# Kernel optimization log

Hardware: AMD Instinct MI355X
Metric: run time of the kernel (lower is better)

## Reference

```python
import jax, jax.numpy as jnp
import numpy as np
from jax import lax

B, H, W = 128, 128, 128
CHANS = [3, 32, 64, 128]   # convolution_structure
F, FH, FW = 128, 16, 16    # n_features, feature map size after 3 maxpools
P = FH * FW                # flatten_feature_size = 256
E, OUT = 32, 53            # expert_output_len, output_len


def _conv(x, w, b):
    # NCHW conv, 3x3, SAME padding, stride 1
    y = lax.conv_general_dilated(x, w, (1, 1), 'SAME',
                                 dimension_numbers=('NCHW', 'OIHW', 'NCHW'))
    return y + b[None, :, None, None]


def _maxpool2(x):
    return lax.reduce_window(x, -jnp.inf, lax.max,
                             (1, 1, 2, 2), (1, 1, 2, 2), 'VALID')


def setup_inputs() -> dict:
    key = jax.random.key(0)
    ks = jax.random.split(key, 16)

    def n(k, shape, fan_in):
        return jax.random.normal(k, shape, jnp.float32) / np.float32(np.sqrt(fan_in))

    inp = {'x': jax.random.normal(ks[0], (B, CHANS[0], H, W), jnp.float32)}
    for i in range(3):
        cin, cout = CHANS[i], CHANS[i + 1]
        inp[f'cw{i + 1}'] = n(ks[1 + i], (cout, cin, 3, 3), cin * 9)
        inp[f'cb{i + 1}'] = jnp.zeros((cout,), jnp.float32)
    inp['Wa'] = n(ks[4], (F, P), P)
    inp['ba'] = jnp.zeros((F,), jnp.float32)
    # per-expert MLP 256 -> 256 -> 128 -> 32 (128 experts, batched)
    inp['ew1'] = n(ks[5], (F, 256, 256), 256)
    inp['eb1'] = jnp.zeros((F, 256), jnp.float32)
    inp['ew2'] = n(ks[6], (F, 256, 128), 256)
    inp['eb2'] = jnp.zeros((F, 128), jnp.float32)
    inp['ew3'] = n(ks[7], (F, 128, E), 128)
    inp['eb3'] = jnp.zeros((F, E), jnp.float32)
    inp['fw'] = n(ks[8], (F * E, OUT), F * E)
    inp['fb'] = jnp.zeros((OUT,), jnp.float32)
    return inp


def reference(x, cw1, cb1, cw2, cb2, cw3, cb3, Wa, ba,
              ew1, eb1, ew2, eb2, ew3, eb3, fw, fb):
    # CNNBlock: (conv3x3 + ReLU + maxpool2) x 3  -> [B, F, 16, 16]
    h = x
    for w, b in ((cw1, cb1), (cw2, cb2), (cw3, cb3)):
        h = _maxpool2(jax.nn.relu(_conv(h, w, b)))
    feat = h.reshape(h.shape[0], F, P)                        # [B, F, 256]

    # AttentionBlock: per-feature scalar gate (attention_value = 1)
    att = jax.nn.sigmoid(jnp.einsum('bfp,fp->bf', feat, Wa) + ba)[:, :, None]

    # Experts: 128 independent gated MLPs, batched as grouped GEMMs
    z = feat * att                                            # input gating
    z = jax.nn.relu(jnp.einsum('bfp,fpq->bfq', z, ew1) + eb1)
    z = jax.nn.relu(jnp.einsum('bfp,fpq->bfq', z, ew2) + eb2)
    z = jnp.einsum('bfp,fpq->bfq', z, ew3) + eb3              # [B, F, 32]

    # outer ReLU over stacked expert outputs, flatten, final dense (att=1)
    z = jax.nn.relu(z).reshape(z.shape[0], -1)                # [B, 4096]
    return z @ fw + fb                                        # [B, 53]
```

## Files before the change

kernel.cpp:

```cpp
#include <hip/hip_runtime.h>
#include <hip/hip_bf16.h>
#include <math.h>

#define NF 128
#define NP 256

typedef __attribute__((ext_vector_type(8))) short bf16x8;
typedef __attribute__((ext_vector_type(4))) short bf16x4;
typedef __attribute__((ext_vector_type(4))) float f32x4;

#define GLOBAL_AS __attribute__((address_space(1)))
#define LDS_AS __attribute__((address_space(3)))

__global__ void __launch_bounds__(256) wpack_k(const float* __restrict__ w,
                                               __hip_bfloat16* __restrict__ wp,
                                               int COUT, int CIN)
{
    int i = blockIdx.x * 256 + threadIdx.x;
    int total = 9 * COUT * CIN;
    if (i >= total) return;
    int o  = i / (COUT * CIN);
    int r  = i - o * (COUT * CIN);
    int co = r / CIN, ci = r - co * CIN;
    wp[i] = __float2bfloat16(w[(size_t)(co * CIN + ci) * 9 + o]);
}

__global__ void __launch_bounds__(256) wpack1_k(const float* __restrict__ w,
                                                __hip_bfloat16* __restrict__ wp1)
{
    int i = blockIdx.x * 256 + threadIdx.x;
    if (i >= 2048) return;
    int s = i >> 10, co = (i >> 5) & 31, k = i & 31;
    int o = s * 8 + (k >> 2), ch = k & 3;
    float v = 0.f;
    if (o < 9 && ch < 3) v = w[(size_t)(co * 3 + ch) * 9 + o];
    wp1[i] = __float2bfloat16(v);
}

__global__ void __launch_bounds__(256) tpack_k(const float* __restrict__ in,
                                               __hip_bfloat16* __restrict__ out,
                                               int P, int Q, int qtiles)
{
    const int f  = blockIdx.y;
    const int pt = blockIdx.x / qtiles, qt = blockIdx.x - pt * qtiles;
    __shared__ float t[32][33];
    const float* src = in + (size_t)f * P * Q;
    __hip_bfloat16* dst = out + (size_t)f * P * Q;
    const int rr = threadIdx.x >> 5, c = threadIdx.x & 31;
    #pragma unroll
    for (int i = 0; i < 4; ++i)
        t[rr + i * 8][c] = src[(size_t)(pt * 32 + rr + i * 8) * Q + qt * 32 + c];
    __syncthreads();
    #pragma unroll
    for (int i = 0; i < 4; ++i)
        dst[(size_t)(qt * 32 + rr + i * 8) * P + pt * 32 + c] =
            __float2bfloat16(t[c][rr + i * 8]);
}

__global__ void __launch_bounds__(256) fwt_k(const float* __restrict__ fw, float* __restrict__ fwt)
{
    int i = blockIdx.x * 256 + threadIdx.x;
    if (i >= 53 * 4096) return;
    int o = i >> 12, k = i & 4095;
    fwt[i] = fw[(size_t)k * 53 + o];
}

__global__ void __launch_bounds__(256, 2) conv1_mfma(
    const float* __restrict__ x,
    const __hip_bfloat16* __restrict__ wp1,
    const float* __restrict__ bias,
    __hip_bfloat16* __restrict__ out)
{
    __shared__ char lds[14 * 130 * 8];
    const int rb  = blockIdx.x * 8;
    const int b   = blockIdx.z;
    const int tid = threadIdx.x;

    #pragma unroll
    for (int t = 0; t < 8; ++t) {
        int u = tid + t * 256;
        if (u < 14 * 130) {
            int px = u % 130, row = u / 130;
            int gy = rb + row - 1, gx = px - 1;
            unsigned short hv[4] = {0, 0, 0, 0};
            if (gy >= 0 && gy < 128 && gx >= 0 && gx < 128) {
                size_t base = (((size_t)b * 3) * 128 + gy) * 128 + gx;
                __hip_bfloat16 h0 = __float2bfloat16(x[base]);
                __hip_bfloat16 h1 = __float2bfloat16(x[base + 16384]);
                __hip_bfloat16 h2 = __float2bfloat16(x[base + 32768]);
                __builtin_memcpy(&hv[0], &h0, 2);
                __builtin_memcpy(&hv[1], &h1, 2);
                __builtin_memcpy(&hv[2], &h2, 2);
            }
            *(int2*)(lds + u * 8) = *(const int2*)hv;
        }
    }
    __syncthreads();

    const int w = tid >> 6, lane = tid & 63, p = lane & 15, q = lane >> 4;

    f32x4 acc[16][2];
    #pragma unroll
    for (int m = 0; m < 16; ++m)
        #pragma unroll
        for (int n = 0; n < 2; ++n) {
            acc[m][n][0] = 0.f; acc[m][n][1] = 0.f;
            acc[m][n][2] = 0.f; acc[m][n][3] = 0.f;
        }

    #pragma unroll
    for (int s = 0; s < 2; ++s) {
        bf16x8 bfr[2];
        #pragma unroll
        for (int n = 0; n < 2; ++n)
            bfr[n] = *(const bf16x8*)(wp1 + (size_t)(s * 32 + n * 16 + p) * 32 + q * 8);
        const int o0 = s * 8 + q * 2, o1 = o0 + 1;
        const int dy0 = o0 / 3, dx0 = o0 - 3 * dy0;
        const int dy1 = o1 / 3, dx1 = o1 - 3 * dy1;
        #pragma unroll
        for (int m = 0; m < 16; ++m) {
            const int mr = m >> 3, mx = m & 7;
            const int r0 = (2 * w + mr + dy0) * 130 + mx * 16 + p + dx0;
            const int r1 = (2 * w + mr + dy1) * 130 + mx * 16 + p + dx1;
            bf16x4 lo = *(const bf16x4*)(lds + r0 * 8);
            bf16x4 hi = *(const bf16x4*)(lds + r1 * 8);
            bf16x8 afr = __builtin_shufflevector(lo, hi, 0, 1, 2, 3, 4, 5, 6, 7);
            #pragma unroll
            for (int n = 0; n < 2; ++n)
                acc[m][n] = __builtin_amdgcn_mfma_f32_16x16x32_bf16(afr, bfr[n], acc[m][n], 0, 0, 0);
        }
    }

    const int prow = (rb >> 1) + w;
    float bv[2] = { bias[p], bias[16 + p] };
    #pragma unroll
    for (int mx = 0; mx < 8; ++mx)
        #pragma unroll
        for (int n = 0; n < 2; ++n) {
            f32x4 lo = acc[mx][n], hi = acc[8 + mx][n];
            float v0 = fmaxf(fmaxf(fmaxf(lo[0], lo[1]), fmaxf(hi[0], hi[1])) + bv[n], 0.f);
            float v1 = fmaxf(fmaxf(fmaxf(lo[2], lo[3]), fmaxf(hi[2], hi[3])) + bv[n], 0.f);
            int px = mx * 8 + q * 2;
            size_t base = ((size_t)(b * 64 + prow) * 64 + px) * 32 + n * 16 + p;
            out[base]      = __float2bfloat16(v0);
            out[base + 32] = __float2bfloat16(v1);
        }
}

template<int W, int CIN, int COUT, int SWZ, int OUTF>
__global__ void __launch_bounds__(256, 2) conv_mfma(
    const __hip_bfloat16* __restrict__ in,
    const __hip_bfloat16* __restrict__ wp,
    const float* __restrict__ bias,
    __hip_bfloat16* __restrict__ outb,
    float* __restrict__ outf)
{
    constexpr int XW  = W / 16;
    constexpr int AF  = 2 * XW;
    constexpr int BF  = COUT / 16;
    constexpr int CH  = CIN / 8;
    constexpr int KH  = CIN / 32;
    constexpr int NSTEP = 9 * KH;
    constexpr int PXW = W + 2;
    constexpr int UNITS  = 10 * PXW * CH;
    constexpr int NIT    = (UNITS + 255) / 256;
    constexpr int STAGEB = UNITS * 16;
    constexpr int OUTLDS = OUTF ? (COUT * 68 * 4) : 0;
    constexpr int LDSB   = STAGEB > OUTLDS ? STAGEB : OUTLDS;

    __shared__ int4 ldsv[(LDSB + 15) / 16];
    char* ldsc = (char*)ldsv;

    const int rb  = blockIdx.x * 8;
    const int b   = blockIdx.z;
    const int tid = threadIdx.x;
    const int w = tid >> 6, lane = tid & 63, p = lane & 15, q = lane >> 4;

    #pragma unroll
    for (int t = 0; t < NIT; ++t) {
        int u = tid + t * 256;
        if (u < UNITS) {
            int ch = u % CH; int pl = u / CH;
            int xx = pl % PXW; int row = pl / PXW;
            int gy = rb + row - 1, gx = xx - 1;
            if (gy >= 0 && gy < W && gx >= 0 && gx < W) {
                int ch_src = SWZ ? (ch ^ (pl & 7)) : ch;
                const __hip_bfloat16* gp = in + ((size_t)(b * W + gy) * W + gx) * CIN + ch_src * 8;
                char* lb = ldsc + (size_t)(t * 256 + (tid & ~63)) * 16;
                __builtin_amdgcn_global_load_lds(
                    (const GLOBAL_AS void*)gp, (LDS_AS void*)lb, 16, 0, 0);
            } else {
                *(int4*)(ldsc + (size_t)u * 16) = make_int4(0, 0, 0, 0);
            }
        }
    }

    bf16x8 bcur[BF], bnxt[BF];
    #pragma unroll
    for (int n = 0; n < BF; ++n)
        bcur[n] = *(const bf16x8*)(wp + (size_t)(n * 16 + p) * CIN + q * 8);

    __syncthreads();

    f32x4 acc[AF][BF];
    #pragma unroll
    for (int m = 0; m < AF; ++m)
        #pragma unroll
        for (int n = 0; n < BF; ++n) {
            acc[m][n][0] = 0.f; acc[m][n][1] = 0.f;
            acc[m][n][2] = 0.f; acc[m][n][3] = 0.f;
        }

    float bv[BF];
    #pragma unroll
    for (int n = 0; n < BF; ++n) bv[n] = bias[n * 16 + p];

    #pragma unroll 1
    for (int s = 0; s < NSTEP; ++s) {
        const int o  = (KH == 1) ? s : (s >> 1);
        const int h  = (KH == 1) ? 0 : (s & 1);
        const int ky = o / 3, kx = o - 3 * (o / 3);

        if (s + 1 < NSTEP) {
            const int o2 = (KH == 1) ? (s + 1) : ((s + 1) >> 1);
            const int h2 = (KH == 1) ? 0 : ((s + 1) & 1);
            #pragma unroll
            for (int n = 0; n < BF; ++n)
                bnxt[n] = *(const bf16x8*)(wp + (size_t)(o2 * COUT + n * 16 + p) * CIN + h2 * 32 + q * 8);
        }

        bf16x8 afr[AF];
        #pragma unroll
        for (int m = 0; m < AF; ++m) {
            const int mr = m / XW, mx = m % XW;
            const int pix = (2 * w + mr + ky) * PXW + mx * 16 + kx + p;
            const int ch = h * 4 + q;
            const int slot = SWZ ? (pix * CH + (ch ^ (pix & 7))) : (pix * CH + ch);
            afr[m] = *(const bf16x8*)(ldsc + slot * 16);
        }
        #pragma unroll
        for (int m = 0; m < AF; ++m)
            #pragma unroll
            for (int n = 0; n < BF; ++n)
                acc[m][n] = __builtin_amdgcn_mfma_f32_16x16x32_bf16(afr[m], bcur[n], acc[m][n], 0, 0, 0);

        #pragma unroll
        for (int n = 0; n < BF; ++n) bcur[n] = bnxt[n];
    }

    const int prow = (rb >> 1) + w;
    if constexpr (OUTF == 0) {
        #pragma unroll
        for (int mx = 0; mx < XW; ++mx)
            #pragma unroll
            for (int n = 0; n < BF; ++n) {
                f32x4 lo = acc[mx][n], hi = acc[XW + mx][n];
                float v0 = fmaxf(fmaxf(fmaxf(lo[0], lo[1]), fmaxf(hi[0], hi[1])) + bv[n], 0.f);
                float v1 = fmaxf(fmaxf(fmaxf(lo[2], lo[3]), fmaxf(hi[2], hi[3])) + bv[n], 0.f);
                int px = mx * 8 + q * 2;
                size_t base = ((size_t)(b * (W / 2) + prow) * (W / 2) + px) * COUT + n * 16 + p;
                outb[base]        = __float2bfloat16(v0);
                outb[base + COUT] = __float2bfloat16(v1);
            }
    } else {
        __syncthreads();
        float* fl = (float*)ldsc;
        #pragma unroll
        for (int mx = 0; mx < XW; ++mx)
            #pragma unroll
            for (int n = 0; n < BF; ++n) {
                f32x4 lo = acc[mx][n], hi = acc[XW + mx][n];
                float v0 = fmaxf(fmaxf(fmaxf(lo[0], lo[1]), fmaxf(hi[0], hi[1])) + bv[n], 0.f);
                float v1 = fmaxf(fmaxf(fmaxf(lo[2], lo[3]), fmaxf(hi[2], hi[3])) + bv[n], 0.f);
                int px = mx * 8 + q * 2;
                fl[(n * 16 + p) * 68 + w * 16 + px]     = v0;
                fl[(n * 16 + p) * 68 + w * 16 + px + 1] = v1;
            }
        __syncthreads();
        for (int i = tid; i < COUT * 16; i += 256) {
            int c = i >> 4, j4 = i & 15;
            float4 vv = *(const float4*)&fl[c * 68 + j4 * 4];
            *(float4*)(outf + (size_t)(b * COUT + c) * 256 + (rb >> 1) * 16 + j4 * 4) = vv;
        }
    }
}

__global__ void __launch_bounds__(256) attention_k(
    const float* __restrict__ feat, const float* __restrict__ Wa,
    const float* __restrict__ ba, float* __restrict__ att)
{
    const int wid  = blockIdx.x * 4 + (threadIdx.x >> 6);
    const int lane = threadIdx.x & 63;
    const int b = wid >> 7, f = wid & 127;

    const float4 a  = ((const float4*)&feat[((size_t)b * NF + f) * NP])[lane];
    const float4 wv = ((const float4*)&Wa[(size_t)f * NP])[lane];
    float s = a.x * wv.x + a.y * wv.y + a.z * wv.z + a.w * wv.w;
    #pragma unroll
    for (int off = 32; off; off >>= 1) s += __shfl_down(s, off);
    if (lane == 0) att[b * NF + f] = 1.f / (1.f + expf(-(s + ba[f])));
}

__global__ void __launch_bounds__(256, 2) experts_mfma(
    const float* __restrict__ feat, const float* __restrict__ att,
    const __hip_bfloat16* __restrict__ w1, const float* __restrict__ eb1,
    const __hip_bfloat16* __restrict__ w2, const float* __restrict__ eb2,
    const __hip_bfloat16* __restrict__ w3, const float* __restrict__ eb3,
    float* __restrict__ z)
{
    const int f  = blockIdx.x;
    const int r0 = blockIdx.y * 32;
    const int tid = threadIdx.x;

    __shared__ char lds[32768];
    char* Xb  = lds;
    char* H1b = lds + 16384;
    char* H2b = lds;

    for (int u = tid; u < 32 * 32; u += 256) {
        int row = u >> 5, ch = u & 31;
        int b = r0 + row;
        const float* src = feat + ((size_t)b * NF + f) * NP + ch * 8;
        float g = att[b * NF + f];
        float4 v0 = *(const float4*)src;
        float4 v1 = *(const float4*)(src + 4);
        unsigned short hv[8];
        float vv[8] = {v0.x, v0.y, v0.z, v0.w, v1.x, v1.y, v1.z, v1.w};
        #pragma unroll
        for (int j = 0; j < 8; ++j) {
            __hip_bfloat16 hb = __float2bfloat16(vv[j] * g);
            __builtin_memcpy(&hv[j], &hb, 2);
        }
        int slot = row * 32 + (ch ^ (row & 7));
        *(int4*)(Xb + slot * 16) = *(const int4*)hv;
    }
    __syncthreads();

    const int wv = tid >> 6, lane = tid & 63, p = lane & 15, q = lane >> 4;
    const int rh = wv & 1, cf = wv >> 1;
    const int mrow = rh * 16;

    f32x4 acc1[8];
    #pragma unroll
    for (int n = 0; n < 8; ++n) { acc1[n][0]=0.f; acc1[n][1]=0.f; acc1[n][2]=0.f; acc1[n][3]=0.f; }
    #pragma unroll
    for (int k = 0; k < 8; ++k) {
        bf16x8 bfr[8];
        #pragma unroll
        for (int n = 0; n < 8; ++n)
            bfr[n] = *(const bf16x8*)(w1 + ((size_t)f * 256 + cf * 128 + n * 16 + p) * 256 + k * 32 + q * 8);
        int row = mrow + p, ch = k * 4 + q;
        bf16x8 afr = *(const bf16x8*)(Xb + (row * 32 + (ch ^ (row & 7))) * 16);
        #pragma unroll
        for (int n = 0; n < 8; ++n)
            acc1[n] = __builtin_amdgcn_mfma_f32_16x16x32_bf16(afr, bfr[n], acc1[n], 0, 0, 0);
    }
    #pragma unroll
    for (int n = 0; n < 8; ++n) {
        int col = cf * 128 + n * 16 + p;
        float bb = eb1[(size_t)f * 256 + col];
        #pragma unroll
        for (int reg = 0; reg < 4; ++reg) {
            float v = fmaxf(acc1[n][reg] + bb, 0.f);
            int row = mrow + q * 4 + reg;
            int slot = row * 32 + ((col >> 3) ^ (row & 7));
            *(__hip_bfloat16*)(H1b + slot * 16 + (col & 7) * 2) = __float2bfloat16(v);
        }
    }
    __syncthreads();

    f32x4 acc2[4];
    #pragma unroll
    for (int n = 0; n < 4; ++n) { acc2[n][0]=0.f; acc2[n][1]=0.f; acc2[n][2]=0.f; acc2[n][3]=0.f; }
    #pragma unroll
    for (int k = 0; k < 8; ++k) {
        bf16x8 bfr[4];
        #pragma unroll
        for (int n = 0; n < 4; ++n)
            bfr[n] = *(const bf16x8*)(w2 + ((size_t)f * 128 + cf * 64 + n * 16 + p) * 256 + k * 32 + q * 8);
        int row = mrow + p, ch = k * 4 + q;
        bf16x8 afr = *(const bf16x8*)(H1b + (row * 32 + (ch ^ (row & 7))) * 16);
        #pragma unroll
        for (int n = 0; n < 4; ++n)
            acc2[n] = __builtin_amdgcn_mfma_f32_16x16x32_bf16(afr, bfr[n], acc2[n], 0, 0, 0);
    }
    #pragma unroll
    for (int n = 0; n < 4; ++n) {
        int col = cf * 64 + n * 16 + p;
        float bb = eb2[(size_t)f * 128 + col];
        #pragma unroll
        for (int reg = 0; reg < 4; ++reg) {
            float v = fmaxf(acc2[n][reg] + bb, 0.f);
            int row = mrow + q * 4 + reg;
            int slot = row * 16 + ((col >> 3) ^ (row & 7));
            *(__hip_bfloat16*)(H2b + slot * 16 + (col & 7) * 2) = __float2bfloat16(v);
        }
    }
    __syncthreads();

    f32x4 acc3;
    acc3[0]=0.f; acc3[1]=0.f; acc3[2]=0.f; acc3[3]=0.f;
    #pragma unroll
    for (int k = 0; k < 4; ++k) {
        bf16x8 bfr = *(const bf16x8*)(w3 + ((size_t)f * 32 + cf * 16 + p) * 128 + k * 32 + q * 8);
        int row = mrow + p, ch = k * 4 + q;
        bf16x8 afr = *(const bf16x8*)(H2b + (row * 16 + (ch ^ (row & 7))) * 16);
        acc3 = __builtin_amdgcn_mfma_f32_16x16x32_bf16(afr, bfr, acc3, 0, 0, 0);
    }
    {
        float bb = eb3[(size_t)f * 32 + cf * 16 + p];
        #pragma unroll
        for (int reg = 0; reg < 4; ++reg) {
            float v = fmaxf(acc3[reg] + bb, 0.f);
            int row = r0 + mrow + q * 4 + reg;
            z[(size_t)row * 4096 + f * 32 + cf * 16 + p] = v;
        }
    }
}

__global__ void __launch_bounds__(256) final_k(
    const float* __restrict__ z, const float* __restrict__ fwt,
    const float* __restrict__ fb, float* __restrict__ out)
{
    const int b  = blockIdx.x;
    const int og = blockIdx.y;
    __shared__ float zs[4096];
    for (int i = threadIdx.x; i < 1024; i += 256)
        *(float4*)&zs[i * 4] = *(const float4*)&z[(size_t)b * 4096 + i * 4];
    __syncthreads();

    const int wv = threadIdx.x >> 6, lane = threadIdx.x & 63;
    const int o = og * 4 + wv;
    if (o >= 53) return;
    const float4* wr = (const float4*)&fwt[(size_t)o * 4096];
    float s = 0.f;
    #pragma unroll
    for (int it = 0; it < 16; ++it) {
        float4 zv = *(const float4*)&zs[(it * 64 + lane) * 4];
        float4 w4 = wr[it * 64 + lane];
        s += zv.x * w4.x + zv.y * w4.y + zv.z * w4.z + zv.w * w4.w;
    }
    #pragma unroll
    for (int off = 32; off; off >>= 1) s += __shfl_down(s, off);
    if (lane == 0) out[b * 53 + o] = s + fb[o];
}

extern "C" void kernel_launch(void* const* d_in, const int* in_sizes, int n_in,
                              void* d_out, int out_size, void* d_ws, size_t ws_size,
                              hipStream_t stream)
{
    const float* x   = (const float*)d_in[0];
    const float* cw1 = (const float*)d_in[1];
    const float* cb1 = (const float*)d_in[2];
    const float* cw2 = (const float*)d_in[3];
    const float* cb2 = (const float*)d_in[4];
    const float* cw3 = (const float*)d_in[5];
    const float* cb3 = (const float*)d_in[6];
    const float* Wa  = (const float*)d_in[7];
    const float* ba  = (const float*)d_in[8];
    const float* ew1 = (const float*)d_in[9];
    const float* eb1 = (const float*)d_in[10];
    const float* ew2 = (const float*)d_in[11];
    const float* eb2 = (const float*)d_in[12];
    const float* ew3 = (const float*)d_in[13];
    const float* eb3 = (const float*)d_in[14];
    const float* fw  = (const float*)d_in[15];
    const float* fb  = (const float*)d_in[16];

    float* ws = (float*)d_ws;
    __hip_bfloat16* p1b  = (__hip_bfloat16*)ws;
    __hip_bfloat16* p2b  = (__hip_bfloat16*)(ws + 8388608);
    float* feat = ws + 12582912;
    float* att  = ws + 16777216;
    __hip_bfloat16* wp2  = (__hip_bfloat16*)(ws + 16793600);
    __hip_bfloat16* wp3  = (__hip_bfloat16*)(ws + 16802816);
    __hip_bfloat16* ew1b = (__hip_bfloat16*)(ws + 16839680);
    __hip_bfloat16* ew2b = (__hip_bfloat16*)(ws + 21033984);
    __hip_bfloat16* ew3b = (__hip_bfloat16*)(ws + 23131136);
    float* fwt = ws + 23393280;
    __hip_bfloat16* wp1b = (__hip_bfloat16*)(ws + 23610368);
    float* z   = ws;

    wpack1_k<<<8, 256, 0, stream>>>(cw1, wp1b);
    wpack_k<<<72, 256, 0, stream>>>(cw2, wp2, 64, 32);
    wpack_k<<<288, 256, 0, stream>>>(cw3, wp3, 128, 64);
    tpack_k<<<dim3(64, 128), 256, 0, stream>>>(ew1, ew1b, 256, 256, 8);
    tpack_k<<<dim3(32, 128), 256, 0, stream>>>(ew2, ew2b, 256, 128, 4);
    tpack_k<<<dim3(4, 128), 256, 0, stream>>>(ew3, ew3b, 128, 32, 1);
    fwt_k<<<848, 256, 0, stream>>>(fw, fwt);

    conv1_mfma<<<dim3(16, 1, 128), 256, 0, stream>>>(x, wp1b, cb1, p1b);
    conv_mfma<64, 32, 64, 0, 0><<<dim3(8, 1, 128), 256, 0, stream>>>(p1b, wp2, cb2, p2b, nullptr);
    conv_mfma<32, 64, 128, 1, 1><<<dim3(4, 1, 128), 256, 0, stream>>>(p2b, wp3, cb3, nullptr, feat);
    attention_k<<<4096, 256, 0, stream>>>(feat, Wa, ba, att);
    experts_mfma<<<dim3(128, 4), 256, 0, stream>>>(feat, att, ew1b, eb1, ew2b, eb2, ew3b, eb3, z);
    final_k<<<dim3(128, 14), 256, 0, stream>>>(z, fwt, fb, (float*)d_out);
}
```

Measured before the change: 161.1 us.

## Fuse attention gate into experts kernel, merge weight packs, raise conv occupancy

Attention gating moves into the experts kernel. Each block computes the sigmoid gate for its 32 rows into LDS and applies it to the first GEMM accumulator rather than scaling the input, which is valid because the gate is a per-row scalar. The three conv weight-pack kernels and the fw transpose are merged into one launch. The conv_mfma launch bound is raised from 2 to 3 blocks per CU. These cut kernel launches and the att round trip through global memory, at the cost of a slightly different bf16 rounding order and possible register spills in conv.

```diff
diff --git a/kernel.cpp b/kernel.cpp
--- a/kernel.cpp
+++ b/kernel.cpp
@@ -12,29 +12,39 @@
 #define GLOBAL_AS __attribute__((address_space(1)))
 #define LDS_AS __attribute__((address_space(3)))
 
-__global__ void __launch_bounds__(256) wpack_k(const float* __restrict__ w,
-                                               __hip_bfloat16* __restrict__ wp,
-                                               int COUT, int CIN)
-{
-    int i = blockIdx.x * 256 + threadIdx.x;
-    int total = 9 * COUT * CIN;
-    if (i >= total) return;
-    int o  = i / (COUT * CIN);
-    int r  = i - o * (COUT * CIN);
-    int co = r / CIN, ci = r - co * CIN;
-    wp[i] = __float2bfloat16(w[(size_t)(co * CIN + ci) * 9 + o]);
-}
-
-__global__ void __launch_bounds__(256) wpack1_k(const float* __restrict__ w,
-                                                __hip_bfloat16* __restrict__ wp1)
-{
-    int i = blockIdx.x * 256 + threadIdx.x;
-    if (i >= 2048) return;
-    int s = i >> 10, co = (i >> 5) & 31, k = i & 31;
-    int o = s * 8 + (k >> 2), ch = k & 3;
-    float v = 0.f;
-    if (o < 9 && ch < 3) v = w[(size_t)(co * 3 + ch) * 9 + o];
-    wp1[i] = __float2bfloat16(v);
+__global__ void __launch_bounds__(256) packs_k(
+    const float* __restrict__ cw1, const float* __restrict__ cw2,
+    const float* __restrict__ cw3, const float* __restrict__ fw,
+    __hip_bfloat16* __restrict__ wp1, __hip_bfloat16* __restrict__ wp2,
+    __hip_bfloat16* __restrict__ wp3, float* __restrict__ fwt)
+{
+    const int bid = blockIdx.x, tid = threadIdx.x;
+    if (bid < 8) {
+        int i = bid * 256 + tid;
+        if (i >= 2048) return;
+        int s = i >> 10, co = (i >> 5) & 31, k = i & 31;
+        int o = s * 8 + (k >> 2), ch = k & 3;
+        float v = 0.f;
+        if (o < 9 && ch < 3) v = cw1[(size_t)(co * 3 + ch) * 9 + o];
+        wp1[i] = __float2bfloat16(v);
+    } else if (bid < 80) {
+        int i = (bid - 8) * 256 + tid;
+        if (i >= 9 * 64 * 32) return;
+        int o = i / 2048, r = i - o * 2048;
+        int co = r >> 5, ci = r & 31;
+        wp2[i] = __float2bfloat16(cw2[(size_t)(co * 32 + ci) * 9 + o]);
+    } else if (bid < 368) {
+        int i = (bid - 80) * 256 + tid;
+        if (i >= 9 * 128 * 64) return;
+        int o = i / 8192, r = i - o * 8192;
+        int co = r >> 6, ci = r & 63;
+        wp3[i] = __float2bfloat16(cw3[(size_t)(co * 64 + ci) * 9 + o]);
+    } else {
+        int i = (bid - 368) * 256 + tid;
+        if (i >= 53 * 4096) return;
+        int o = i >> 12, k = i & 4095;
+        fwt[i] = fw[(size_t)k * 53 + o];
+    }
 }
 
 __global__ void __launch_bounds__(256) tpack_k(const float* __restrict__ in,
@@ -55,14 +65,6 @@
     for (int i = 0; i < 4; ++i)
         dst[(size_t)(qt * 32 + rr + i * 8) * P + pt * 32 + c] =
             __float2bfloat16(t[c][rr + i * 8]);
-}
-
-__global__ void __launch_bounds__(256) fwt_k(const float* __restrict__ fw, float* __restrict__ fwt)
-{
-    int i = blockIdx.x * 256 + threadIdx.x;
-    if (i >= 53 * 4096) return;
-    int o = i >> 12, k = i & 4095;
-    fwt[i] = fw[(size_t)k * 53 + o];
 }
 
 __global__ void __launch_bounds__(256, 2) conv1_mfma(
@@ -148,7 +150,7 @@
 }
 
 template<int W, int CIN, int COUT, int SWZ, int OUTF>
-__global__ void __launch_bounds__(256, 2) conv_mfma(
+__global__ void __launch_bounds__(256, 3) conv_mfma(
     const __hip_bfloat16* __restrict__ in,
     const __hip_bfloat16* __restrict__ wp,
     const float* __restrict__ bias,
@@ -285,24 +287,9 @@
     }
 }
 
-__global__ void __launch_bounds__(256) attention_k(
+__global__ void __launch_bounds__(256, 2) experts_mfma(
     const float* __restrict__ feat, const float* __restrict__ Wa,
-    const float* __restrict__ ba, float* __restrict__ att)
-{
-    const int wid  = blockIdx.x * 4 + (threadIdx.x >> 6);
-    const int lane = threadIdx.x & 63;
-    const int b = wid >> 7, f = wid & 127;
-
-    const float4 a  = ((const float4*)&feat[((size_t)b * NF + f) * NP])[lane];
-    const float4 wv = ((const float4*)&Wa[(size_t)f * NP])[lane];
-    float s = a.x * wv.x + a.y * wv.y + a.z * wv.z + a.w * wv.w;
-    #pragma unroll
-    for (int off = 32; off; off >>= 1) s += __shfl_down(s, off);
-    if (lane == 0) att[b * NF + f] = 1.f / (1.f + expf(-(s + ba[f])));
-}
-
-__global__ void __launch_bounds__(256, 2) experts_mfma(
-    const float* __restrict__ feat, const float* __restrict__ att,
+    const float* __restrict__ ba,
     const __hip_bfloat16* __restrict__ w1, const float* __restrict__ eb1,
     const __hip_bfloat16* __restrict__ w2, const float* __restrict__ eb2,
     const __hip_bfloat16* __restrict__ w3, const float* __restrict__ eb3,
@@ -312,27 +299,44 @@
     const int r0 = blockIdx.y * 32;
     const int tid = threadIdx.x;
 
-    __shared__ char lds[32768];
+    __shared__ __attribute__((aligned(16))) char lds[33024];
     char* Xb  = lds;
     char* H1b = lds + 16384;
     char* H2b = lds;
+    float* attL = (float*)(lds + 32768);
 
     for (int u = tid; u < 32 * 32; u += 256) {
         int row = u >> 5, ch = u & 31;
         int b = r0 + row;
         const float* src = feat + ((size_t)b * NF + f) * NP + ch * 8;
-        float g = att[b * NF + f];
         float4 v0 = *(const float4*)src;
         float4 v1 = *(const float4*)(src + 4);
         unsigned short hv[8];
         float vv[8] = {v0.x, v0.y, v0.z, v0.w, v1.x, v1.y, v1.z, v1.w};
         #pragma unroll
         for (int j = 0; j < 8; ++j) {
-            __hip_bfloat16 hb = __float2bfloat16(vv[j] * g);
+            __hip_bfloat16 hb = __float2bfloat16(vv[j]);
             __builtin_memcpy(&hv[j], &hb, 2);
         }
         int slot = row * 32 + (ch ^ (row & 7));
         *(int4*)(Xb + slot * 16) = *(const int4*)hv;
+    }
+
+    {
+        int row = tid >> 3, g = tid & 7;
+        const float* fr = feat + ((size_t)(r0 + row) * NF + f) * NP + g * 32;
+        const float* wr = Wa + (size_t)f * NP + g * 32;
+        float s = 0.f;
+        #pragma unroll
+        for (int j = 0; j < 32; j += 4) {
+            float4 a  = *(const float4*)(fr + j);
+            float4 w4 = *(const float4*)(wr + j);
+            s += a.x * w4.x + a.y * w4.y + a.z * w4.z + a.w * w4.w;
+        }
+        s += __shfl_xor(s, 1);
+        s += __shfl_xor(s, 2);
+        s += __shfl_xor(s, 4);
+        if (g == 0) attL[row] = 1.f / (1.f + expf(-(s + ba[f])));
     }
     __syncthreads();
 
@@ -361,8 +365,8 @@
         float bb = eb1[(size_t)f * 256 + col];
         #pragma unroll
         for (int reg = 0; reg < 4; ++reg) {
-            float v = fmaxf(acc1[n][reg] + bb, 0.f);
             int row = mrow + q * 4 + reg;
+            float v = fmaxf(attL[row] * acc1[n][reg] + bb, 0.f);
             int slot = row * 32 + ((col >> 3) ^ (row & 7));
             *(__hip_bfloat16*)(H1b + slot * 16 + (col & 7) * 2) = __float2bfloat16(v);
         }
@@ -471,7 +475,6 @@
     __hip_bfloat16* p1b  = (__hip_bfloat16*)ws;
     __hip_bfloat16* p2b  = (__hip_bfloat16*)(ws + 8388608);
     float* feat = ws + 12582912;
-    float* att  = ws + 16777216;
     __hip_bfloat16* wp2  = (__hip_bfloat16*)(ws + 16793600);
     __hip_bfloat16* wp3  = (__hip_bfloat16*)(ws + 16802816);
     __hip_bfloat16* ew1b = (__hip_bfloat16*)(ws + 16839680);
@@ -481,18 +484,14 @@
     __hip_bfloat16* wp1b = (__hip_bfloat16*)(ws + 23610368);
     float* z   = ws;
 
-    wpack1_k<<<8, 256, 0, stream>>>(cw1, wp1b);
-    wpack_k<<<72, 256, 0, stream>>>(cw2, wp2, 64, 32);
-    wpack_k<<<288, 256, 0, stream>>>(cw3, wp3, 128, 64);
+    packs_k<<<1216, 256, 0, stream>>>(cw1, cw2, cw3, fw, wp1b, wp2, wp3, fwt);
     tpack_k<<<dim3(64, 128), 256, 0, stream>>>(ew1, ew1b, 256, 256, 8);
     tpack_k<<<dim3(32, 128), 256, 0, stream>>>(ew2, ew2b, 256, 128, 4);
     tpack_k<<<dim3(4, 128), 256, 0, stream>>>(ew3, ew3b, 128, 32, 1);
-    fwt_k<<<848, 256, 0, stream>>>(fw, fwt);
 
     conv1_mfma<<<dim3(16, 1, 128), 256, 0, stream>>>(x, wp1b, cb1, p1b);
     conv_mfma<64, 32, 64, 0, 0><<<dim3(8, 1, 128), 256, 0, stream>>>(p1b, wp2, cb2, p2b, nullptr);
     conv_mfma<32, 64, 128, 1, 1><<<dim3(4, 1, 128), 256, 0, stream>>>(p2b, wp3, cb3, nullptr, feat);
-    attention_k<<<4096, 256, 0, stream>>>(feat, Wa, ba, att);
-    experts_mfma<<<dim3(128, 4), 256, 0, stream>>>(feat, att, ew1b, eb1, ew2b, eb2, ew3b, eb3, z);
+    experts_mfma<<<dim3(128, 4), 256, 0, stream>>>(feat, Wa, ba, ew1b, eb1, ew2b, eb2, ew3b, eb3, z);
     final_k<<<dim3(128, 14), 256, 0, stream>>>(z, fwt, fb, (float*)d_out);
 }
```

Measured after the change: 221.1 us. 1.37x slower.
